# Performance work log

Measured on AMD Instinct MI355X. Metric: run time of the kernel, lower is better.

## Reference

```python
import jax, jax.numpy as jnp
import numpy as np

B, R, N, D = 8, 5, 1024, 512  # batch, relations, utterances per dialogue, d_model
LN_EPS = 1e-5


def setup_inputs() -> dict:
    key = jax.random.key(0)
    k1, k2, k3 = jax.random.split(key, 3)
    h = jax.random.normal(k1, (B, N, D), dtype=jnp.float32)
    # Binary adjacency: adj[b, r, v, u] = 1 means u sends a message to v under relation r.
    adj = (jax.random.uniform(k2, (B, R, N, N)) < 0.5).astype(jnp.float32)
    # Relation 0 is the self-loop relation (identity), as in build_adjacency.
    adj = adj.at[:, 0].set(jnp.broadcast_to(jnp.eye(N, dtype=jnp.float32), (B, N, N)))
    # Per-relation Linear (bias=False) weights, torch convention: y = x @ W_r.T, W_r: (D, D)
    W = jax.random.normal(k3, (R, D, D), dtype=jnp.float32) * 0.02
    gamma = jnp.ones((D,), dtype=jnp.float32)
    beta = jnp.zeros((D,), dtype=jnp.float32)
    return {"h": h, "adj": adj, "W": W, "gamma": gamma, "beta": beta}


def reference(h, adj, W, gamma, beta):
    # Degree-normalize each relation's adjacency (row-normalized mean aggregation).
    deg = jnp.clip(jnp.sum(adj, axis=-1, keepdims=True), 1.0)  # (B,R,N,1)
    A = adj / deg
    # Mean aggregation per relation: (B,R,N,N) @ (B,N,D) -> (B,R,N,D)
    msg = jnp.einsum('brvu,bud->brvd', A, h)
    # Per-relation linear (x @ W_r.T) and sum over relations: (B,N,D)
    agg = jnp.einsum('brvd,red->bve', msg, W)
    # Dropout is identity in eval mode; ReLU, residual, LayerNorm.
    out = jax.nn.relu(agg) + h
    mu = jnp.mean(out, axis=-1, keepdims=True)
    xc = out - mu
    var = jnp.mean(xc * xc, axis=-1, keepdims=True)
    return xc / jnp.sqrt(var + LN_EPS) * gamma + beta
```

## Files before the change

kernel.cpp:

```cpp
#include <hip/hip_runtime.h>
#include <stdint.h>

#define Bd 8
#define Rr 5
#define Nn 1024
#define Dd 512
#define KK (Rr*Dd)

typedef __attribute__((ext_vector_type(8))) short bf16x8;
typedef __attribute__((ext_vector_type(4))) float f32x4;
typedef unsigned short u16;
typedef unsigned int u32;

__device__ __forceinline__ u16 f2bf(float x){
  union { float f; unsigned u; } v; v.f = x;
  unsigned r = v.u + 0x7FFFu + ((v.u >> 16) & 1u);
  return (u16)(r >> 16);
}

__device__ __forceinline__ void gll16(const void* g, void* l){
  __builtin_amdgcn_global_load_lds(
      (const __attribute__((address_space(1))) void*)g,
      (__attribute__((address_space(3))) void*)l, 16, 0, 0);
}

__global__ __launch_bounds__(256) void k_prep(
    const float* __restrict__ h, const float* __restrict__ W,
    u16* __restrict__ hTp, u16* __restrict__ Wt2, u16* __restrict__ msg){
  __shared__ float t32[32][65];
  const int tid = threadIdx.x;
  const int g = blockIdx.x;
  if (g < 2048){
    const int ut  = g & 31;
    const int dtg = (g >> 5) & 7;
    const int b   = g >> 8;
    const float* hb = h + ((size_t)b*Nn + (size_t)ut*32)*Dd + dtg*64;
    #pragma unroll
    for (int j=0;j<8;j++){
      int e = j*256 + tid;
      int ul = e >> 6, dl = e & 63;
      t32[ul][dl] = hb[(size_t)ul*Dd + dl];
    }
    __syncthreads();
    u16* ob = hTp + (size_t)b*Dd*Nn;
    #pragma unroll
    for (int j=0;j<8;j++){
      int e = j*256 + tid;
      int dtl = e >> 9;
      int rem = e & 511;
      int dr = rem >> 5, uu = rem & 31;
      int dt = dtg*4 + dtl;
      ob[((size_t)ut*32 + dt)*512 + rem] = f2bf(t32[uu][dtl*16 + dr]);
    }
  } else if (g < 3328){
    int idx = (g - 2048)*1024 + tid*4;
    int e = idx / KK;
    int k = idx % KK;
    int ri = (k < 2048) ? (1 + (k >> 9)) : 0;
    int d = k & 511;
    f32x4 w = *(const f32x4*)(W + (((size_t)ri*Dd + e)*Dd + d));
    u16 o[4] = { f2bf(w.x), f2bf(w.y), f2bf(w.z), f2bf(w.w) };
    *(uint2*)(Wt2 + idx) = *(uint2*)o;
  } else {
    int q = g - 3328;
    int row = q*4 + (tid >> 6);
    int d0 = (tid & 63)*8;
    f32x4 a = *(const f32x4*)(h + (size_t)row*Dd + d0);
    f32x4 c = *(const f32x4*)(h + (size_t)row*Dd + d0 + 4);
    bf16x8 pk;
    pk[0]=(short)f2bf(a.x); pk[1]=(short)f2bf(a.y);
    pk[2]=(short)f2bf(a.z); pk[3]=(short)f2bf(a.w);
    pk[4]=(short)f2bf(c.x); pk[5]=(short)f2bf(c.y);
    pk[6]=(short)f2bf(c.z); pk[7]=(short)f2bf(c.w);
    *(bf16x8*)(msg + (size_t)row*KK + 2048 + d0) = pk;
  }
}

__global__ __launch_bounds__(512,2) void k_msg(
    const float* __restrict__ adj, const u16* __restrict__ hTp,
    u16* __restrict__ msg){
  __shared__ __align__(16) u16 sA[2][4][16*64];
  __shared__ float sT[16*516];
  __shared__ float sDeg[4][16];

  const int tid  = threadIdx.x;
  const int lane = tid & 63;
  const int wave = tid >> 6;
  const int bid = blockIdx.x;
  const int b  = bid & 7;
  const int vt = bid >> 3;
  const int v0 = vt * 16;
  const int t0 = bid & 15;
  const float* adjb = adj + (((size_t)b*Rr + 1)*Nn + v0)*Nn;
  const u16* hTpb = hTp + (size_t)b*Dd*Nn;

  const int ari = tid >> 7;
  const int srow = (tid >> 3) & 15;
  const int sc   = tid & 7;
  const size_t aoff = (size_t)ari*Nn*Nn + (size_t)srow*Nn + sc*8;
  const int wslot = sc ^ (srow & 7);

  float deg = 0.f;
  f32x4 ar0, ar1;
  f32x4 acc[4][4];
  #pragma unroll
  for (int ri=0;ri<4;ri++)
    #pragma unroll
    for (int n=0;n<4;n++) acc[ri][n] = (f32x4){0.f,0.f,0.f,0.f};

  const int rlo = lane & 15, ch = lane >> 4;
  const int boff = rlo*32 + ch*8;

  #define TT(x) (((x) + t0) & 15)

  #define AISSUE(T) do {                                                      \
    const float* _ap = adjb + (size_t)(T)*64 + aoff;                          \
    ar0 = *(const f32x4*)_ap;                                                 \
    ar1 = *(const f32x4*)(_ap + 4);                                           \
  } while(0)

  #define PACK(BUFI) do {                                                     \
    deg += ar0.x+ar0.y+ar0.z+ar0.w + ar1.x+ar1.y+ar1.z+ar1.w;                 \
    uint4 pk;                             \
    pk.x = (__float_as_uint(ar0.x)>>16) | (__float_as_uint(ar0.y) & 0xFFFF0000u);\
    pk.y = (__float_as_uint(ar0.z)>>16) | (__float_as_uint(ar0.w) & 0xFFFF0000u);\
    pk.z = (__float_as_uint(ar1.x)>>16) | (__float_as_uint(ar1.y) & 0xFFFF0000u);\
    pk.w = (__float_as_uint(ar1.z)>>16) | (__float_as_uint(ar1.w) & 0xFFFF0000u);\
    *(uint4*)((char*)sA[BUFI][ari] + srow*128 + (wslot<<4)) = pk;             \
  } while(0)

  #define LOADB(T) do {                                                      \
    _Pragma("unroll")                                                         \
    for (int kk=0;kk<2;kk++){                                                 \
      const u16* bp = hTpb + ((((size_t)((T)*2+kk))*32 + (wave<<2))<<9) + boff;\
      _Pragma("unroll")                                                       \
      for (int n=0;n<4;n++)                                                   \
        bfr[kk][n] = *(const bf16x8*)(bp + ((size_t)n<<9));                   \
    }                                                                         \
  } while(0)

  #define MSTEP(BUFI) do {                                                    \
    const char* abase = (const char*)sA[BUFI];                                \
    _Pragma("unroll")                                                         \
    for (int kk=0;kk<2;kk++){                                                 \
      _Pragma("unroll")                                                       \
      for (int ri=0;ri<4;ri++){                                               \
        const int row = rlo;                                                  \
        bf16x8 af = *(const bf16x8*)(abase + ri*2048 + row*128                \
                  + (((kk*4 + ch) ^ (row&7))<<4));                            \
        _Pragma("unroll")                                                     \
        for (int n=0;n<4;n++)                                                 \
          acc[ri][n] = __builtin_amdgcn_mfma_f32_16x16x32_bf16(               \
              af, bfr[kk][n], acc[ri][n], 0, 0, 0);                           \
      }                                                                       \
    }                                                                         \
  } while(0)

  #define FENCE() __builtin_amdgcn_sched_barrier(0)
  #define STEP_BARRIER() do {                                                 \
    asm volatile("s_waitcnt lgkmcnt(0)" ::: "memory");                        \
    FENCE();                                                                  \
    __builtin_amdgcn_s_barrier();                                             \
    FENCE();                                                                  \
  } while(0)

  bf16x8 bfr[2][4];

  AISSUE(TT(0));
  PACK(0);
  __syncthreads();
  LOADB(TT(0));
  FENCE();
  AISSUE(TT(1));
  FENCE();

  for (int t = 0; t < 15; ++t){
    PACK((t+1)&1);
    FENCE();
    if (t < 14) AISSUE(TT(t+2));
    FENCE();
    MSTEP(t&1);
    FENCE();
    LOADB(TT(t+1));
    STEP_BARRIER();
  }
  MSTEP(1);
  #undef TT
  #undef AISSUE
  #undef PACK
  #undef LOADB
  #undef MSTEP

  {
    float d = deg;
    d += __shfl_xor(d, 1); d += __shfl_xor(d, 2); d += __shfl_xor(d, 4);
    if (sc == 0) sDeg[ari][srow] = d;
  }
  __syncthreads();

  u16* mb = msg + ((size_t)b*Nn + v0)*KK;
  #pragma unroll
  for (int ri=0;ri<4;ri++){
    #pragma unroll
    for (int reg=0;reg<4;reg++){
      const int rl = ch*4 + reg;
      const float inv = 1.0f / fmaxf(sDeg[ri][rl], 1.0f);
      #pragma unroll
      for (int n=0;n<4;n++){
        const int col = (wave<<6) + n*16 + rlo;
        const int colw = col ^ (((col>>5)&7)<<2);
        sT[rl*516 + colw] = acc[ri][n][reg] * inv;
      }
    }
    __syncthreads();
    #pragma unroll
    for (int s=0;s<2;s++){
      const int rl = wave*2 + s;
      const int m5 = lane >> 2;
      const int e  = m5 & 7;
      const int j0 = (2*lane) & 7;
      f32x4 lo = *(const f32x4*)&sT[rl*516 + (m5<<5) + (((j0  ) ^ e)<<2)];
      f32x4 hi = *(const f32x4*)&sT[rl*516 + (m5<<5) + (((j0+1) ^ e)<<2)];
      bf16x8 pk;
      pk[0]=(short)f2bf(lo.x); pk[1]=(short)f2bf(lo.y);
      pk[2]=(short)f2bf(lo.z); pk[3]=(short)f2bf(lo.w);
      pk[4]=(short)f2bf(hi.x); pk[5]=(short)f2bf(hi.y);
      pk[6]=(short)f2bf(hi.z); pk[7]=(short)f2bf(hi.w);
      *(bf16x8*)(mb + (size_t)rl*KK + ri*512 + lane*8) = pk;
    }
    __syncthreads();
  }
  #undef FENCE
  #undef STEP_BARRIER
}

__global__ __launch_bounds__(512,4) void k_agg(
    const u16* __restrict__ msg, const u16* __restrict__ Wt,
    float* __restrict__ agg){
  __shared__ __align__(16) u16 sA[2][64*64];
  __shared__ __align__(16) u16 sB[2][128*64];
  const int tid = threadIdx.x;
  const int lane = tid & 63, wave = tid >> 6;
  const int wm = wave >> 2, wn = wave & 3;
  const int g = blockIdx.x;
  const int et = g >> 7;
  const int bv = g & 127;
  const int b  = bv >> 4;
  const int vt = bv & 15;
  const int v0 = vt*64, e0 = et*128;
  const u16* Ab = msg + ((size_t)b*Nn + v0)*KK;
  const u16* Bb = Wt + (size_t)e0*KK;

  f32x4 acc[2][2];
  #pragma unroll
  for (int m=0;m<2;m++)
    #pragma unroll
    for (int n=0;n<2;n++) acc[m][n] = (f32x4){0.f,0.f,0.f,0.f};

  #define STAGE(buf, kt) do {                                              \
    { int c = tid; int row_ = c>>3, chg = (c&7) ^ (row_&7);                \
      gll16(Ab + (size_t)row_*KK + (kt)*64 + chg*8,                        \
            (char*)sA[buf] + ((size_t)(wave<<6))*16); }                    \
    _Pragma("unroll")                                                      \
    for (int i=0;i<2;i++){                                                 \
      int c = i*512 + tid; int row_ = c>>3, chg = (c&7) ^ (row_&7);        \
      gll16(Bb + (size_t)row_*KK + (kt)*64 + chg*8,                        \
            (char*)sB[buf] + ((size_t)(i*512 + (wave<<6)))*16);            \
    }                                                                      \
  } while(0)

  STAGE(0, 0);
  __syncthreads();

  const int ch = lane >> 4, rlo = lane & 15;

  for (int kt = 0; kt < KK/64; ++kt){
    if (kt < KK/64 - 1) STAGE((kt+1)&1, kt+1);
    const char* a  = (const char*)sA[kt&1];
    const char* bb = (const char*)sB[kt&1];
    #pragma unroll
    for (int kk=0; kk<2; ++kk){
      bf16x8 af[2], bfx[2];
      #pragma unroll
      for (int m=0;m<2;m++){
        const int row = wm*32 + m*16 + rlo;
        af[m] = *(const bf16x8*)(a + row*128 + ((((kk<<2)+ch) ^ (row&7))<<4));
      }
      #pragma unroll
      for (int n=0;n<2;n++){
        const int row = wn*32 + n*16 + rlo;
        bfx[n] = *(const bf16x8*)(bb + row*128 + ((((kk<<2)+ch) ^ (row&7))<<4));
      }
      #pragma unroll
      for (int m=0;m<2;m++)
        #pragma unroll
        for (int n=0;n<2;n++)
          acc[m][n] = __builtin_amdgcn_mfma_f32_16x16x32_bf16(af[m], bfx[n], acc[m][n], 0, 0, 0);
    }
    __syncthreads();
  }
  #undef STAGE

  float* ob = agg + ((size_t)b*Nn + v0)*Dd + e0;
  #pragma unroll
  for (int m=0;m<2;m++)
    #pragma unroll
    for (int reg=0;reg<4;reg++){
      const int row = wm*32 + m*16 + ((lane>>4)<<2) + reg;
      #pragma unroll
      for (int n=0;n<2;n++){
        const int col = wn*32 + n*16 + (lane & 15);
        ob[(size_t)row*Dd + col] = acc[m][n][reg];
      }
    }
}

__global__ __launch_bounds__(256,4) void k_ln(
    const float* __restrict__ agg, const float* __restrict__ h,
    const float* __restrict__ gamma, const float* __restrict__ beta,
    float* __restrict__ out){
  const int row = blockIdx.x*4 + (threadIdx.x >> 6);
  const int lane = threadIdx.x & 63;
  const float* a  = agg + (size_t)row*Dd;
  const float* hh = h   + (size_t)row*Dd;
  float x[8];
  float sum = 0.f, sq = 0.f;
  #pragma unroll
  for (int q=0;q<2;q++){
    f32x4 av = *(const f32x4*)(a  + ((size_t)q*64+lane)*4);
    f32x4 hv = *(const f32x4*)(hh + ((size_t)q*64+lane)*4);
    #pragma unroll
    for (int k=0;k<4;k++){
      float v = fmaxf(av[k], 0.f) + hv[k];
      x[q*4+k] = v; sum += v; sq += v*v;
    }
  }
  #pragma unroll
  for (int off=32; off; off>>=1){
    sum += __shfl_xor(sum, off);
    sq  += __shfl_xor(sq,  off);
  }
  const float mu  = sum * (1.f/(float)Dd);
  const float var = sq * (1.f/(float)Dd) - mu*mu;
  const float rstd = rsqrtf(var + 1e-5f);
  float* o = out + (size_t)row*Dd;
  #pragma unroll
  for (int q=0;q<2;q++){
    f32x4 g  = *(const f32x4*)(gamma + ((size_t)q*64+lane)*4);
    f32x4 be = *(const f32x4*)(beta  + ((size_t)q*64+lane)*4);
    f32x4 ov;
    #pragma unroll
    for (int k=0;k<4;k++)
      ov[k] = (x[q*4+k] - mu) * rstd * g[k] + be[k];
    *(f32x4*)(o + ((size_t)q*64+lane)*4) = ov;
  }
}

extern "C" void kernel_launch(void* const* d_in, const int* in_sizes, int n_in,
                              void* d_out, int out_size, void* d_ws, size_t ws_size,
                              hipStream_t stream){
  const float* h     = (const float*)d_in[0];
  const float* adj   = (const float*)d_in[1];
  const float* W     = (const float*)d_in[2];
  const float* gamma = (const float*)d_in[3];
  const float* beta  = (const float*)d_in[4];
  float* out = (float*)d_out;
  char* ws = (char*)d_ws;

  u16*  hTp = (u16*)(ws);
  u16*  Wt2 = (u16*)(ws + 8388608);
  u16*  msg = (u16*)(ws + 11010048);
  float* agg = (float*)(ws + 52953088);

  k_prep<<<dim3(5376), dim3(256), 0, stream>>>(h, W, hTp, Wt2, msg);
  k_msg <<<dim3(512), dim3(512), 0, stream>>>(adj, hTp, msg);
  k_agg <<<dim3(Bd*(Nn/64)*(Dd/128)), dim3(512), 0, stream>>>(msg, Wt2, agg);
  k_ln  <<<dim3(Bd*Nn/4), dim3(256), 0, stream>>>(agg, h, gamma, beta, out);
}
```

Baseline: 105.8 us.

## Reassociate to project h by W first, then fuse adjacency aggregation with LayerNorm

The computation is reordered as A·(h·W_rᵀ) instead of (A·h)·W_rᵀ. A GEMM now precomputes G_r = h·W_rᵀ per batch and relation in bf16, in a layout shaped for the fused kernel. A single fused kernel then streams the adjacency through LDS via global_load_lds with triple buffering, accumulates the relation products with degree normalisation, adds the self-loop term, and applies ReLU, the residual and LayerNorm in place. This removes the large msg intermediate, the fp32 agg round-trip and one launch. In exchange, G is rounded to bf16, and the fused kernel uses 1024-thread blocks with 256 blocks and about 128KB of LDS, which limits occupancy.

```diff
diff --git a/kernel.cpp b/kernel.cpp
--- a/kernel.cpp
+++ b/kernel.cpp
@@ -5,7 +5,6 @@
 #define Rr 5
 #define Nn 1024
 #define Dd 512
-#define KK (Rr*Dd)
 
 typedef __attribute__((ext_vector_type(8))) short bf16x8;
 typedef __attribute__((ext_vector_type(4))) float f32x4;
@@ -24,232 +23,39 @@
       (__attribute__((address_space(3))) void*)l, 16, 0, 0);
 }
 
-__global__ __launch_bounds__(256) void k_prep(
+__global__ __launch_bounds__(256) void kc(
     const float* __restrict__ h, const float* __restrict__ W,
-    u16* __restrict__ hTp, u16* __restrict__ Wt2, u16* __restrict__ msg){
-  __shared__ float t32[32][65];
-  const int tid = threadIdx.x;
-  const int g = blockIdx.x;
-  if (g < 2048){
-    const int ut  = g & 31;
-    const int dtg = (g >> 5) & 7;
-    const int b   = g >> 8;
-    const float* hb = h + ((size_t)b*Nn + (size_t)ut*32)*Dd + dtg*64;
-    #pragma unroll
-    for (int j=0;j<8;j++){
-      int e = j*256 + tid;
-      int ul = e >> 6, dl = e & 63;
-      t32[ul][dl] = hb[(size_t)ul*Dd + dl];
-    }
-    __syncthreads();
-    u16* ob = hTp + (size_t)b*Dd*Nn;
-    #pragma unroll
-    for (int j=0;j<8;j++){
-      int e = j*256 + tid;
-      int dtl = e >> 9;
-      int rem = e & 511;
-      int dr = rem >> 5, uu = rem & 31;
-      int dt = dtg*4 + dtl;
-      ob[((size_t)ut*32 + dt)*512 + rem] = f2bf(t32[uu][dtl*16 + dr]);
-    }
-  } else if (g < 3328){
-    int idx = (g - 2048)*1024 + tid*4;
-    int e = idx / KK;
-    int k = idx % KK;
-    int ri = (k < 2048) ? (1 + (k >> 9)) : 0;
-    int d = k & 511;
-    f32x4 w = *(const f32x4*)(W + (((size_t)ri*Dd + e)*Dd + d));
-    u16 o[4] = { f2bf(w.x), f2bf(w.y), f2bf(w.z), f2bf(w.w) };
-    *(uint2*)(Wt2 + idx) = *(uint2*)o;
-  } else {
-    int q = g - 3328;
-    int row = q*4 + (tid >> 6);
-    int d0 = (tid & 63)*8;
-    f32x4 a = *(const f32x4*)(h + (size_t)row*Dd + d0);
-    f32x4 c = *(const f32x4*)(h + (size_t)row*Dd + d0 + 4);
-    bf16x8 pk;
-    pk[0]=(short)f2bf(a.x); pk[1]=(short)f2bf(a.y);
-    pk[2]=(short)f2bf(a.z); pk[3]=(short)f2bf(a.w);
-    pk[4]=(short)f2bf(c.x); pk[5]=(short)f2bf(c.y);
-    pk[6]=(short)f2bf(c.z); pk[7]=(short)f2bf(c.w);
-    *(bf16x8*)(msg + (size_t)row*KK + 2048 + d0) = pk;
-  }
-}
-
-__global__ __launch_bounds__(512,2) void k_msg(
-    const float* __restrict__ adj, const u16* __restrict__ hTp,
-    u16* __restrict__ msg){
-  __shared__ __align__(16) u16 sA[2][4][16*64];
-  __shared__ float sT[16*516];
-  __shared__ float sDeg[4][16];
-
-  const int tid  = threadIdx.x;
-  const int lane = tid & 63;
-  const int wave = tid >> 6;
-  const int bid = blockIdx.x;
-  const int b  = bid & 7;
-  const int vt = bid >> 3;
-  const int v0 = vt * 16;
-  const int t0 = bid & 15;
-  const float* adjb = adj + (((size_t)b*Rr + 1)*Nn + v0)*Nn;
-  const u16* hTpb = hTp + (size_t)b*Dd*Nn;
-
-  const int ari = tid >> 7;
-  const int srow = (tid >> 3) & 15;
-  const int sc   = tid & 7;
-  const size_t aoff = (size_t)ari*Nn*Nn + (size_t)srow*Nn + sc*8;
-  const int wslot = sc ^ (srow & 7);
-
-  float deg = 0.f;
-  f32x4 ar0, ar1;
-  f32x4 acc[4][4];
-  #pragma unroll
-  for (int ri=0;ri<4;ri++)
-    #pragma unroll
-    for (int n=0;n<4;n++) acc[ri][n] = (f32x4){0.f,0.f,0.f,0.f};
-
-  const int rlo = lane & 15, ch = lane >> 4;
-  const int boff = rlo*32 + ch*8;
-
-  #define TT(x) (((x) + t0) & 15)
-
-  #define AISSUE(T) do {                                                      \
-    const float* _ap = adjb + (size_t)(T)*64 + aoff;                          \
-    ar0 = *(const f32x4*)_ap;                                                 \
-    ar1 = *(const f32x4*)(_ap + 4);                                           \
-  } while(0)
-
-  #define PACK(BUFI) do {                                                     \
-    deg += ar0.x+ar0.y+ar0.z+ar0.w + ar1.x+ar1.y+ar1.z+ar1.w;                 \
-    uint4 pk;                             \
-    pk.x = (__float_as_uint(ar0.x)>>16) | (__float_as_uint(ar0.y) & 0xFFFF0000u);\
-    pk.y = (__float_as_uint(ar0.z)>>16) | (__float_as_uint(ar0.w) & 0xFFFF0000u);\
-    pk.z = (__float_as_uint(ar1.x)>>16) | (__float_as_uint(ar1.y) & 0xFFFF0000u);\
-    pk.w = (__float_as_uint(ar1.z)>>16) | (__float_as_uint(ar1.w) & 0xFFFF0000u);\
-    *(uint4*)((char*)sA[BUFI][ari] + srow*128 + (wslot<<4)) = pk;             \
-  } while(0)
-
-  #define LOADB(T) do {                                                      \
-    _Pragma("unroll")                                                         \
-    for (int kk=0;kk<2;kk++){                                                 \
-      const u16* bp = hTpb + ((((size_t)((T)*2+kk))*32 + (wave<<2))<<9) + boff;\
-      _Pragma("unroll")                                                       \
-      for (int n=0;n<4;n++)                                                   \
-        bfr[kk][n] = *(const bf16x8*)(bp + ((size_t)n<<9));                   \
-    }                                                                         \
-  } while(0)
-
-  #define MSTEP(BUFI) do {                                                    \
-    const char* abase = (const char*)sA[BUFI];                                \
-    _Pragma("unroll")                                                         \
-    for (int kk=0;kk<2;kk++){                                                 \
-      _Pragma("unroll")                                                       \
-      for (int ri=0;ri<4;ri++){                                               \
-        const int row = rlo;                                                  \
-        bf16x8 af = *(const bf16x8*)(abase + ri*2048 + row*128                \
-                  + (((kk*4 + ch) ^ (row&7))<<4));                            \
-        _Pragma("unroll")                                                     \
-        for (int n=0;n<4;n++)                                                 \
-          acc[ri][n] = __builtin_amdgcn_mfma_f32_16x16x32_bf16(               \
-              af, bfr[kk][n], acc[ri][n], 0, 0, 0);                           \
-      }                                                                       \
-    }                                                                         \
-  } while(0)
-
-  #define FENCE() __builtin_amdgcn_sched_barrier(0)
-  #define STEP_BARRIER() do {                                                 \
-    asm volatile("s_waitcnt lgkmcnt(0)" ::: "memory");                        \
-    FENCE();                                                                  \
-    __builtin_amdgcn_s_barrier();                                             \
-    FENCE();                                                                  \
-  } while(0)
-
-  bf16x8 bfr[2][4];
-
-  AISSUE(TT(0));
-  PACK(0);
-  __syncthreads();
-  LOADB(TT(0));
-  FENCE();
-  AISSUE(TT(1));
-  FENCE();
-
-  for (int t = 0; t < 15; ++t){
-    PACK((t+1)&1);
-    FENCE();
-    if (t < 14) AISSUE(TT(t+2));
-    FENCE();
-    MSTEP(t&1);
-    FENCE();
-    LOADB(TT(t+1));
-    STEP_BARRIER();
-  }
-  MSTEP(1);
-  #undef TT
-  #undef AISSUE
-  #undef PACK
-  #undef LOADB
-  #undef MSTEP
-
-  {
-    float d = deg;
-    d += __shfl_xor(d, 1); d += __shfl_xor(d, 2); d += __shfl_xor(d, 4);
-    if (sc == 0) sDeg[ari][srow] = d;
-  }
-  __syncthreads();
-
-  u16* mb = msg + ((size_t)b*Nn + v0)*KK;
-  #pragma unroll
-  for (int ri=0;ri<4;ri++){
-    #pragma unroll
-    for (int reg=0;reg<4;reg++){
-      const int rl = ch*4 + reg;
-      const float inv = 1.0f / fmaxf(sDeg[ri][rl], 1.0f);
-      #pragma unroll
-      for (int n=0;n<4;n++){
-        const int col = (wave<<6) + n*16 + rlo;
-        const int colw = col ^ (((col>>5)&7)<<2);
-        sT[rl*516 + colw] = acc[ri][n][reg] * inv;
-      }
-    }
-    __syncthreads();
-    #pragma unroll
-    for (int s=0;s<2;s++){
-      const int rl = wave*2 + s;
-      const int m5 = lane >> 2;
-      const int e  = m5 & 7;
-      const int j0 = (2*lane) & 7;
-      f32x4 lo = *(const f32x4*)&sT[rl*516 + (m5<<5) + (((j0  ) ^ e)<<2)];
-      f32x4 hi = *(const f32x4*)&sT[rl*516 + (m5<<5) + (((j0+1) ^ e)<<2)];
-      bf16x8 pk;
-      pk[0]=(short)f2bf(lo.x); pk[1]=(short)f2bf(lo.y);
-      pk[2]=(short)f2bf(lo.z); pk[3]=(short)f2bf(lo.w);
-      pk[4]=(short)f2bf(hi.x); pk[5]=(short)f2bf(hi.y);
-      pk[6]=(short)f2bf(hi.z); pk[7]=(short)f2bf(hi.w);
-      *(bf16x8*)(mb + (size_t)rl*KK + ri*512 + lane*8) = pk;
-    }
-    __syncthreads();
-  }
-  #undef FENCE
-  #undef STEP_BARRIER
-}
-
-__global__ __launch_bounds__(512,4) void k_agg(
-    const u16* __restrict__ msg, const u16* __restrict__ Wt,
-    float* __restrict__ agg){
+    u16* __restrict__ hb, u16* __restrict__ Wb){
+  const int g = blockIdx.x, tid = threadIdx.x;
+  const float* src; u16* dst; size_t idx;
+  if (g < 2048){ idx = (size_t)g*2048 + tid*8; src = h; dst = hb; }
+  else         { idx = (size_t)(g-2048)*2048 + tid*8; src = W; dst = Wb; }
+  f32x4 a = *(const f32x4*)(src + idx);
+  f32x4 c = *(const f32x4*)(src + idx + 4);
+  bf16x8 pk;
+  pk[0]=(short)f2bf(a.x); pk[1]=(short)f2bf(a.y);
+  pk[2]=(short)f2bf(a.z); pk[3]=(short)f2bf(a.w);
+  pk[4]=(short)f2bf(c.x); pk[5]=(short)f2bf(c.y);
+  pk[6]=(short)f2bf(c.z); pk[7]=(short)f2bf(c.w);
+  *(bf16x8*)(dst + idx) = pk;
+}
+
+__global__ __launch_bounds__(512,4) void k_gr(
+    const u16* __restrict__ hb, const u16* __restrict__ Wb,
+    u16* __restrict__ Gp){
   __shared__ __align__(16) u16 sA[2][64*64];
   __shared__ __align__(16) u16 sB[2][128*64];
   const int tid = threadIdx.x;
   const int lane = tid & 63, wave = tid >> 6;
   const int wm = wave >> 2, wn = wave & 3;
   const int g = blockIdx.x;
-  const int et = g >> 7;
-  const int bv = g & 127;
-  const int b  = bv >> 4;
-  const int vt = bv & 15;
-  const int v0 = vt*64, e0 = et*128;
-  const u16* Ab = msg + ((size_t)b*Nn + v0)*KK;
-  const u16* Bb = Wt + (size_t)e0*KK;
+  const int utb = g & 7;
+  const int etb = (g >> 3) & 7;
+  const int br = g >> 6;
+  const int r = br % 5;
+  const int b = br / 5;
+  const u16* Ab = Wb + ((size_t)r*512 + etb*64)*512;
+  const u16* Bb = hb + ((size_t)b*1024 + utb*128)*512;
 
   f32x4 acc[2][2];
   #pragma unroll
@@ -259,12 +65,12 @@
 
   #define STAGE(buf, kt) do {                                              \
     { int c = tid; int row_ = c>>3, chg = (c&7) ^ (row_&7);                \
-      gll16(Ab + (size_t)row_*KK + (kt)*64 + chg*8,                        \
+      gll16(Ab + (size_t)row_*512 + (kt)*64 + chg*8,                       \
             (char*)sA[buf] + ((size_t)(wave<<6))*16); }                    \
     _Pragma("unroll")                                                      \
     for (int i=0;i<2;i++){                                                 \
       int c = i*512 + tid; int row_ = c>>3, chg = (c&7) ^ (row_&7);        \
-      gll16(Bb + (size_t)row_*KK + (kt)*64 + chg*8,                        \
+      gll16(Bb + (size_t)row_*512 + (kt)*64 + chg*8,                       \
             (char*)sB[buf] + ((size_t)(i*512 + (wave<<6)))*16);            \
     }                                                                      \
   } while(0)
@@ -274,8 +80,8 @@
 
   const int ch = lane >> 4, rlo = lane & 15;
 
-  for (int kt = 0; kt < KK/64; ++kt){
-    if (kt < KK/64 - 1) STAGE((kt+1)&1, kt+1);
+  for (int kt = 0; kt < 8; ++kt){
+    if (kt < 7) STAGE((kt+1)&1, kt+1);
     const char* a  = (const char*)sA[kt&1];
     const char* bb = (const char*)sB[kt&1];
     #pragma unroll
@@ -301,59 +107,216 @@
   }
   #undef STAGE
 
-  float* ob = agg + ((size_t)b*Nn + v0)*Dd + e0;
   #pragma unroll
   for (int m=0;m<2;m++)
     #pragma unroll
     for (int reg=0;reg<4;reg++){
-      const int row = wm*32 + m*16 + ((lane>>4)<<2) + reg;
+      const int e = etb*64 + wm*32 + m*16 + ((lane>>4)<<2) + reg;
       #pragma unroll
       for (int n=0;n<2;n++){
-        const int col = wn*32 + n*16 + (lane & 15);
-        ob[(size_t)row*Dd + col] = acc[m][n][reg];
+        const int u = utb*128 + wn*32 + n*16 + (lane & 15);
+        Gp[(((size_t)b*32 + (u>>5))*160 + r*32 + (e>>4))*512
+           + (size_t)((e&15)*32 + (u&31))] = f2bf(acc[m][n][reg]);
       }
     }
 }
 
-__global__ __launch_bounds__(256,4) void k_ln(
-    const float* __restrict__ agg, const float* __restrict__ h,
-    const float* __restrict__ gamma, const float* __restrict__ beta,
-    float* __restrict__ out){
-  const int row = blockIdx.x*4 + (threadIdx.x >> 6);
-  const int lane = threadIdx.x & 63;
-  const float* a  = agg + (size_t)row*Dd;
-  const float* hh = h   + (size_t)row*Dd;
-  float x[8];
-  float sum = 0.f, sq = 0.f;
-  #pragma unroll
-  for (int q=0;q<2;q++){
-    f32x4 av = *(const f32x4*)(a  + ((size_t)q*64+lane)*4);
-    f32x4 hv = *(const f32x4*)(hh + ((size_t)q*64+lane)*4);
-    #pragma unroll
-    for (int k=0;k<4;k++){
-      float v = fmaxf(av[k], 0.f) + hv[k];
-      x[q*4+k] = v; sum += v; sq += v*v;
+__global__ __launch_bounds__(1024,4) void k_fuse(
+    const float* __restrict__ adj, const u16* __restrict__ Gp,
+    const float* __restrict__ h, const float* __restrict__ gamma,
+    const float* __restrict__ beta, float* __restrict__ out){
+  __shared__ __align__(16) char smem[131584];
+  char* sAc = smem + 98304;
+  float (*sDeg)[32] = (float(*)[32])(smem + 131072);
+  float* sT = (float*)smem;
+
+  const int tid  = threadIdx.x;
+  const int lane = tid & 63;
+  const int wave = tid >> 6;
+  const int b  = blockIdx.x & 7;
+  const int vt = blockIdx.x >> 3;
+  const int v0 = vt * 32;
+  const int t0 = blockIdx.x & 15;
+  const float* adjb = adj + (((size_t)b*Rr + 1)*Nn + v0)*Nn;
+  const u16* Gpb = Gp + (size_t)b*32*160*512;
+
+  const int pari  = tid >> 8;
+  const int psrow = ((tid>>5)&7)*4 + ((tid&31)>>3);
+  const int psc   = tid & 7;
+  const int pwslot = psc ^ (psrow & 7);
+
+  const int rlo = lane & 15, ch = lane >> 4;
+  const int boff = rlo*32 + ch*8;
+
+  float deg = 0.f;
+  f32x4 accr[4][2][2];
+  f32x4 acct[2][2];
+  #pragma unroll
+  for (int ri=0;ri<4;ri++)
+    #pragma unroll
+    for (int m=0;m<2;m++)
+      #pragma unroll
+      for (int n=0;n<2;n++) accr[ri][m][n] = (f32x4){0.f,0.f,0.f,0.f};
+
+  #pragma unroll
+  for (int m=0;m<2;m++)
+    #pragma unroll
+    for (int n=0;n<2;n++)
+      #pragma unroll
+      for (int reg=0;reg<4;reg++){
+        u16 gv = Gpb[((size_t)vt*160 + (wave*2+m))*512 + (ch*4+reg)*32 + n*16 + rlo];
+        acct[m][n][reg] = __uint_as_float((u32)gv << 16);
+      }
+
+  #define TT(x) (((x) + t0) & 15)
+
+  #define GLLA(T) do {                                                        \
+    char* _d = smem + ((T)%3)*32768 + (size_t)wave*2048;                      \
+    _Pragma("unroll")                                                         \
+    for (int s_=0;s_<2;s_++){                                                 \
+      const int g_ = wave*2 + s_;                                             \
+      gll16(adjb + (size_t)(g_>>3)*Nn*Nn                                      \
+                 + (size_t)((g_&7)*4 + (lane>>4))*Nn + TT(T)*64 + (lane&15)*4,\
+            _d + s_*1024);                                                    \
+    }                                                                         \
+  } while(0)
+
+  #define PACKL(T) do {                                                      \
+    const float* _s = (const float*)(smem + ((T)%3)*32768 + (size_t)tid*32);  \
+    f32x4 p0 = *(const f32x4*)_s;                                             \
+    f32x4 p1 = *(const f32x4*)(_s + 4);                                       \
+    deg += p0.x+p0.y+p0.z+p0.w + p1.x+p1.y+p1.z+p1.w;                         \
+    uint4 pk;                             \
+    pk.x = (__float_as_uint(p0.x)>>16) | (__float_as_uint(p0.y) & 0xFFFF0000u);\
+    pk.y = (__float_as_uint(p0.z)>>16) | (__float_as_uint(p0.w) & 0xFFFF0000u);\
+    pk.z = (__float_as_uint(p1.x)>>16) | (__float_as_uint(p1.y) & 0xFFFF0000u);\
+    pk.w = (__float_as_uint(p1.z)>>16) | (__float_as_uint(p1.w) & 0xFFFF0000u);\
+    *(uint4*)(sAc + ((T)&1)*16384 + pari*4096 + psrow*128 + (pwslot<<4)) = pk; \
+  } while(0)
+
+  #define MSTEP(T) do {                                                       \
+    const char* abase = sAc + ((T)&1)*16384;                                  \
+    _Pragma("unroll")                                                         \
+    for (int kk=0;kk<2;kk++){                                                 \
+      const size_t gut_ = (size_t)(TT(T)*2 + kk);                             \
+      _Pragma("unroll")                                                       \
+      for (int ri=0;ri<4;ri++){                                               \
+        const u16* gp = Gpb + (gut_*160 + (ri+1)*32 + wave*2)*512 + boff;     \
+        bf16x8 aG0 = *(const bf16x8*)gp;                                      \
+        bf16x8 aG1 = *(const bf16x8*)(gp + 512);                              \
+        bf16x8 bv0 = *(const bf16x8*)(abase + ri*4096 + rlo*128               \
+                      + (((kk*4+ch) ^ (rlo&7))<<4));                          \
+        bf16x8 bv1 = *(const bf16x8*)(abase + ri*4096 + (16+rlo)*128          \
+                      + (((kk*4+ch) ^ (rlo&7))<<4));                          \
+        accr[ri][0][0] = __builtin_amdgcn_mfma_f32_16x16x32_bf16(aG0, bv0, accr[ri][0][0], 0,0,0); \
+        accr[ri][0][1] = __builtin_amdgcn_mfma_f32_16x16x32_bf16(aG0, bv1, accr[ri][0][1], 0,0,0); \
+        accr[ri][1][0] = __builtin_amdgcn_mfma_f32_16x16x32_bf16(aG1, bv0, accr[ri][1][0], 0,0,0); \
+        accr[ri][1][1] = __builtin_amdgcn_mfma_f32_16x16x32_bf16(aG1, bv1, accr[ri][1][1], 0,0,0); \
+      }                                                                       \
+    }                                                                         \
+  } while(0)
+
+  #define FENCE() __builtin_amdgcn_sched_barrier(0)
+  #define STEP_BARRIER() do {                                                 \
+    asm volatile("s_waitcnt lgkmcnt(0)" ::: "memory");                        \
+    FENCE();                                                                  \
+    __builtin_amdgcn_s_barrier();                                             \
+    FENCE();                                                                  \
+  } while(0)
+
+  GLLA(0);
+  GLLA(1);
+  asm volatile("s_waitcnt vmcnt(2)" ::: "memory");
+  FENCE();
+  PACKL(0);
+  __syncthreads();
+
+  for (int t = 0; t < 15; ++t){
+    MSTEP(t);
+    FENCE();
+    if (t < 14) GLLA(t+2);
+    FENCE();
+    PACKL(t+1);
+    STEP_BARRIER();
+  }
+  MSTEP(15);
+  #undef TT
+  #undef GLLA
+  #undef PACKL
+  #undef MSTEP
+
+  {
+    float d = deg;
+    d += __shfl_xor(d, 1); d += __shfl_xor(d, 2); d += __shfl_xor(d, 4);
+    if (psc == 0) sDeg[pari][psrow] = d;
+  }
+  __syncthreads();
+
+  #pragma unroll
+  for (int ri=0;ri<4;ri++)
+    #pragma unroll
+    for (int n=0;n<2;n++){
+      const float inv = 1.0f / fmaxf(sDeg[ri][n*16 + rlo], 1.0f);
+      #pragma unroll
+      for (int m=0;m<2;m++)
+        #pragma unroll
+        for (int reg=0;reg<4;reg++)
+          acct[m][n][reg] += accr[ri][m][n][reg] * inv;
     }
+  __syncthreads();
+
+  #pragma unroll
+  for (int n=0; n<2; ++n){
+    #pragma unroll
+    for (int m=0;m<2;m++)
+      #pragma unroll
+      for (int reg=0;reg<4;reg++){
+        const int e = wave*32 + m*16 + ch*4 + reg;
+        const int colw = e ^ (((e>>5)&7)<<2);
+        sT[rlo*516 + colw] = fmaxf(acct[m][n][reg], 0.f);
+      }
+    __syncthreads();
+    {
+      const int grow = v0 + n*16 + wave;
+      const float* hp = h + ((size_t)b*Nn + grow)*Dd + lane*8;
+      float x[8];
+      float sum = 0.f, sq = 0.f;
+      #pragma unroll
+      for (int j=0;j<2;j++){
+        const int col = lane*8 + j*4;
+        const int colw = col ^ (((col>>5)&7)<<2);
+        f32x4 sv = *(const f32x4*)&sT[wave*516 + colw];
+        f32x4 hv = *(const f32x4*)(hp + j*4);
+        #pragma unroll
+        for (int k=0;k<4;k++){
+          float val = sv[k] + hv[k];
+          x[j*4+k] = val; sum += val; sq += val*val;
+        }
+      }
+      #pragma unroll
+      for (int off=32; off; off>>=1){
+        sum += __shfl_xor(sum, off);
+        sq  += __shfl_xor(sq,  off);
+      }
+      const float mu  = sum * (1.f/(float)Dd);
+      const float var = sq * (1.f/(float)Dd) - mu*mu;
+      const float rstd = rsqrtf(var + 1e-5f);
+      float* op = out + ((size_t)b*Nn + grow)*Dd + lane*8;
+      #pragma unroll
+      for (int j=0;j<2;j++){
+        f32x4 g  = *(const f32x4*)(gamma + lane*8 + j*4);
+        f32x4 be = *(const f32x4*)(beta  + lane*8 + j*4);
+        f32x4 ov;
+        #pragma unroll
+        for (int k=0;k<4;k++)
+          ov[k] = (x[j*4+k] - mu) * rstd * g[k] + be[k];
+        *(f32x4*)(op + j*4) = ov;
+      }
+    }
+    __syncthreads();
   }
-  #pragma unroll
-  for (int off=32; off; off>>=1){
-    sum += __shfl_xor(sum, off);
-    sq  += __shfl_xor(sq,  off);
-  }
-  const float mu  = sum * (1.f/(float)Dd);
-  const float var = sq * (1.f/(float)Dd) - mu*mu;
-  const float rstd = rsqrtf(var + 1e-5f);
-  float* o = out + (size_t)row*Dd;
-  #pragma unroll
-  for (int q=0;q<2;q++){
-    f32x4 g  = *(const f32x4*)(gamma + ((size_t)q*64+lane)*4);
-    f32x4 be = *(const f32x4*)(beta  + ((size_t)q*64+lane)*4);
-    f32x4 ov;
-    #pragma unroll
-    for (int k=0;k<4;k++)
-      ov[k] = (x[q*4+k] - mu) * rstd * g[k] + be[k];
-    *(f32x4*)(o + ((size_t)q*64+lane)*4) = ov;
-  }
+  #undef FENCE
+  #undef STEP_BARRIER
 }
 
 extern "C" void kernel_launch(void* const* d_in, const int* in_sizes, int n_in,
@@ -367,13 +330,11 @@
   float* out = (float*)d_out;
   char* ws = (char*)d_ws;
 
-  u16*  hTp = (u16*)(ws);
-  u16*  Wt2 = (u16*)(ws + 8388608);
-  u16*  msg = (u16*)(ws + 11010048);
-  float* agg = (float*)(ws + 52953088);
-
-  k_prep<<<dim3(5376), dim3(256), 0, stream>>>(h, W, hTp, Wt2, msg);
-  k_msg <<<dim3(512), dim3(512), 0, stream>>>(adj, hTp, msg);
-  k_agg <<<dim3(Bd*(Nn/64)*(Dd/128)), dim3(512), 0, stream>>>(msg, Wt2, agg);
-  k_ln  <<<dim3(Bd*Nn/4), dim3(256), 0, stream>>>(agg, h, gamma, beta, out);
-}
+  u16* hb = (u16*)(ws);
+  u16* Wb = (u16*)(ws + 8388608);
+  u16* Gp = (u16*)(ws + 11010048);
+
+  kc    <<<dim3(2688), dim3(256), 0, stream>>>(h, W, hb, Wb);
+  k_gr  <<<dim3(2560), dim3(512), 0, stream>>>(hb, Wb, Gp);
+  k_fuse<<<dim3(Bd*32), dim3(1024), 0, stream>>>(adj, Gp, h, gamma, beta, out);
+}
```

Result: slower. 124.4 us (+17.5%).
